# Optimization experiments

Measured on AMD Instinct MI355X. Metric: run time of the kernel, lower is better.

The kernel has to match this reference:

```python
import jax, jax.numpy as jnp
import numpy as np

N_NODES = 75000
N_EDGES = 1200000
IN_FEATS = 64
OUT_FEATS = 64


def setup_inputs() -> dict:
    key = jax.random.key(0)
    k1, k2, k3, k4, k5 = jax.random.split(key, 5)
    feature = jax.random.normal(k1, (N_NODES, IN_FEATS), dtype=jnp.float32)
    src = jax.random.randint(k2, (N_EDGES,), 0, N_NODES, dtype=jnp.int32)
    dst = jax.random.randint(k3, (N_EDGES,), 0, N_NODES, dtype=jnp.int32)
    # degree: in-degree + 1 (clamped >= 1 so sqrt/div are well-defined), float32 node data
    deg = np.bincount(np.asarray(dst), minlength=N_NODES).astype(np.float32) + 1.0
    degree = jnp.asarray(deg)
    W = jax.random.normal(k4, (IN_FEATS, OUT_FEATS), dtype=jnp.float32) * (1.0 / np.sqrt(IN_FEATS))
    b = jax.random.normal(k5, (OUT_FEATS,), dtype=jnp.float32) * 0.01
    return {"feature": feature, "degree": degree, "src": src, "dst": dst, "W": W, "b": b}


def reference(feature, degree, src, dst, W, b):
    # message: m_e = h[src_e] / sqrt(degree[src_e])   -> [E, F]
    inv_sqrt_deg = 1.0 / jnp.sqrt(degree)
    m = feature[src] * inv_sqrt_deg[src][:, None]
    # reduce: sum messages into destination nodes      -> [N, F]
    agg = jax.ops.segment_sum(m, dst, num_segments=feature.shape[0])
    # node apply: h = (agg / sqrt(degree)) @ W + b     -> [N, O]
    h = agg * inv_sqrt_deg[:, None]
    return h @ W + b
```

## Files before the change

### kernel.cpp

```cpp
#include <hip/hip_runtime.h>

#define FEATS 64
#define PSZ   64
#define MAXP  1280
#define PSCH  2344
#define SPT   512
#define PEPT  5
#define NBMAX 512
#define CAPP  2560

typedef __attribute__((ext_vector_type(8))) short short8;
typedef __attribute__((ext_vector_type(4))) float floatx4;

static __device__ __forceinline__ unsigned short f2bf(float f) {
    const unsigned int u = __float_as_uint(f);
    return (unsigned short)((u + 0x7FFFu + ((u >> 16) & 1u)) >> 16);
}
static __device__ __forceinline__ float bflo(unsigned int u) {
    return __uint_as_float(u << 16);
}
static __device__ __forceinline__ float bfhi(unsigned int u) {
    return __uint_as_float(u & 0xFFFF0000u);
}

__global__ __launch_bounds__(SPT) void prep_scatter(
        const float* __restrict__ degree,
        const float* __restrict__ feature,
        const float* __restrict__ Wm,
        const int* __restrict__ src,
        const int* __restrict__ dst,
        unsigned short* __restrict__ Fs16,
        unsigned short* __restrict__ WtB,
        int* __restrict__ slab,
        unsigned short* __restrict__ runoff,
        int n_nodes, int n_edges, int np, int rows_per) {
    __shared__ int cnt[MAXP];
    __shared__ int ssum[SPT];
    __shared__ int sval[PSCH];
    const int tid = threadIdx.x;
    const int b = blockIdx.x;

    for (int i = tid; i < np; i += SPT) cnt[i] = 0;

    {
        const int r0 = b * rows_per;
        const int r1 = min(r0 + rows_per, n_nodes);
        for (int idx = r0 * FEATS + tid; idx < r1 * FEATS; idx += SPT) {
            const float w = rsqrtf(degree[idx >> 6]);
            Fs16[idx] = f2bf(feature[idx] * w);
        }
        if (b == 0) {
            if (tid < FEATS) Fs16[(size_t)n_nodes * FEATS + tid] = 0;
            for (int idx = tid; idx < FEATS * FEATS; idx += SPT) {
                const int k = idx >> 6, n = idx & 63;
                WtB[n * FEATS + k] = f2bf(Wm[idx]);
            }
        }
    }
    __syncthreads();

    const int estart = b * PSCH;
    const int eend = min(estart + PSCH, n_edges);
    const int mb = eend - estart;

    int prk[PEPT];
#pragma unroll
    for (int k = 0; k < PEPT; ++k) {
        const int e = estart + tid + k * SPT;
        prk[k] = 0;
        if (e < eend) {
            const int d = dst[e];
            const int p = d >> 6;
            const int r = atomicAdd(&cnt[p], 1);
            prk[k] = p | (r << 11) | ((d & 63) << 23);
        }
    }
    __syncthreads();

    int my[3];
    int psum = 0;
    const int p0 = tid * 3;
#pragma unroll
    for (int j = 0; j < 3; ++j) {
        const int p = p0 + j;
        my[j] = psum;
        if (p < np) psum += cnt[p];
    }
    ssum[tid] = psum;
    __syncthreads();
#pragma unroll
    for (int o = 1; o < SPT; o <<= 1) {
        const int v = (tid >= o) ? ssum[tid - o] : 0;
        __syncthreads();
        ssum[tid] += v;
        __syncthreads();
    }
    const int tbase = ssum[tid] - psum;
#pragma unroll
    for (int j = 0; j < 3; ++j) {
        const int p = p0 + j;
        if (p < np) cnt[p] = tbase + my[j];
    }
    __syncthreads();

#pragma unroll
    for (int k = 0; k < PEPT; ++k) {
        const int e = estart + tid + k * SPT;
        if (e < eend) {
            const int pr = prk[k];
            const int p = pr & 2047;
            const int r = (pr >> 11) & 4095;
            const int dl = (pr >> 23) & 63;
            sval[cnt[p] + r] = (src[e] & 0x1FFFF) | (dl << 17);
        }
    }
    __syncthreads();

    int* so = slab + estart;
    for (int i = tid; i < mb; i += SPT) so[i] = sval[i];
    unsigned short* ro = runoff + (size_t)b * (np + 1);
    for (int i = tid; i <= np; i += SPT)
        ro[i] = (unsigned short)((i < np) ? cnt[i] : mb);
}

__global__ __launch_bounds__(256) void gather_apply5(
        const int* __restrict__ slab,
        const unsigned short* __restrict__ runoff,
        const float* __restrict__ degree,
        const unsigned short* __restrict__ Fs16,
        const unsigned short* __restrict__ WtB,
        const float* __restrict__ bias,
        float* __restrict__ out,
        int n_nodes, int np, int nbs) {
    __shared__ __align__(16) int ledges[CAPP];
    __shared__ __align__(16) unsigned short saggb[PSZ * 72];
    __shared__ int boffA[PSZ + 1];
    __shared__ int bcnt[PSZ];
    __shared__ int bcur[PSZ];
    __shared__ float swinv[PSZ];

    const int tid = threadIdx.x;
    const int lane = tid & 63;
    const int wv = tid >> 6;
    const int p = blockIdx.x;
    const int n0 = p * PSZ;
    const int nn = min(PSZ, n_nodes - n0);

    if (tid < PSZ) bcur[tid] = 0;
    if (wv == 0) {
        const float dg = (lane < nn) ? degree[n0 + lane] : 1.0f;
        swinv[lane] = rsqrtf(dg);
        const int c = (lane < nn) ? ((int)(dg + 0.5f) - 1) : 0;
        const int cp = (c + 7) & ~7;
        int x = cp;
#pragma unroll
        for (int off = 1; off < 64; off <<= 1) {
            const int v = __shfl_up(x, off);
            if (lane >= off) x += v;
        }
        if (lane == 0) boffA[0] = 0;
        boffA[lane + 1] = x;
        bcnt[lane] = c;
    }
    __syncthreads();
    const int mpad = boffA[PSZ];
    const uint2* FsU2 = (const uint2*)Fs16;

    if (mpad <= CAPP) {
        for (int i = tid; i < mpad; i += 256) ledges[i] = n_nodes;
        __syncthreads();
        for (int rr = tid; rr < nbs; rr += 256) {
            const unsigned short* ro = runoff + (size_t)rr * (np + 1);
            const int st = ro[p];
            const int en = ro[p + 1];
            const int* g = slab + (size_t)rr * PSCH;
            for (int q = st; q < en; ++q) {
                const int rec = g[q];
                const int dl = (rec >> 17) & 63;
                const int pos = boffA[dl] + atomicAdd(&bcur[dl], 1);
                ledges[pos] = rec & 0x1FFFF;
            }
        }
        __syncthreads();

        const int q4 = lane >> 4;
        const int c16 = lane & 15;
        for (int n = wv; n < PSZ; n += 4) {
            const int st = boffA[n];
            const int en8 = boffA[n + 1];
            float a0 = 0.f, a1 = 0.f, a2 = 0.f, a3 = 0.f;
            float c0 = 0.f, c1 = 0.f, c2 = 0.f, c3 = 0.f;
#pragma unroll 2
            for (int j = st; j < en8; j += 8) {
                const int r0 = ledges[j + q4];
                const int r1 = ledges[j + 4 + q4];
                const uint2 u0 = FsU2[((size_t)r0 << 4) + c16];
                const uint2 u1 = FsU2[((size_t)r1 << 4) + c16];
                a0 += bflo(u0.x); a1 += bfhi(u0.x);
                a2 += bflo(u0.y); a3 += bfhi(u0.y);
                c0 += bflo(u1.x); c1 += bfhi(u1.x);
                c2 += bflo(u1.y); c3 += bfhi(u1.y);
            }
            float v0 = a0 + c0, v1 = a1 + c1, v2 = a2 + c2, v3 = a3 + c3;
            v0 += __shfl(v0, lane ^ 16); v0 += __shfl(v0, lane ^ 32);
            v1 += __shfl(v1, lane ^ 16); v1 += __shfl(v1, lane ^ 32);
            v2 += __shfl(v2, lane ^ 16); v2 += __shfl(v2, lane ^ 32);
            v3 += __shfl(v3, lane ^ 16); v3 += __shfl(v3, lane ^ 32);
            if (q4 == 0) {
                const unsigned int pk0 =
                    (unsigned int)f2bf(v0) | ((unsigned int)f2bf(v1) << 16);
                const unsigned int pk1 =
                    (unsigned int)f2bf(v2) | ((unsigned int)f2bf(v3) << 16);
                uint2* dp = (uint2*)(saggb + n * 72 + c16 * 4);
                *dp = make_uint2(pk0, pk1);
            }
        }
    } else {
        __syncthreads();
        __syncthreads();
        for (int n = wv; n < PSZ; n += 4) {
            float acc = 0.f;
            for (int t = 0; t < nbs; ++t) {
                const unsigned short* ro = runoff + (size_t)t * (np + 1);
                const int gb = t * PSCH;
                const int e0 = ro[p + 1];
                for (int i = ro[p]; i < e0; ++i) {
                    const int rec = slab[gb + i];
                    if (((rec >> 17) & 63) == n) {
                        const unsigned int us =
                            Fs16[((size_t)(rec & 0x1FFFF) << 6) + lane];
                        acc += __uint_as_float(us << 16);
                    }
                }
            }
            saggb[n * 72 + lane] = f2bf(acc);
        }
    }
    __syncthreads();

    const int col = lane & 15;
    const int quad = lane >> 4;
    floatx4 acc[4] = {};
#pragma unroll
    for (int kt = 0; kt < 2; ++kt) {
        const short8 af = *(const short8*)(saggb + (wv * 16 + col) * 72 + kt * 32 + quad * 8);
#pragma unroll
        for (int nt = 0; nt < 4; ++nt) {
            const short8 bf = *(const short8*)((const short*)WtB + (nt * 16 + col) * FEATS + kt * 32 + quad * 8);
            acc[nt] = __builtin_amdgcn_mfma_f32_16x16x32_bf16(af, bf, acc[nt], 0, 0, 0);
        }
    }
#pragma unroll
    for (int nt = 0; nt < 4; ++nt) {
        const float bv = bias[nt * 16 + col];
#pragma unroll
        for (int r = 0; r < 4; ++r) {
            const int row = wv * 16 + quad * 4 + r;
            if (row < nn)
                out[(size_t)(n0 + row) * FEATS + nt * 16 + col] = swinv[row] * acc[nt][r] + bv;
        }
    }
}

static inline size_t align256(size_t x) { return (x + 255) & ~(size_t)255; }

extern "C" void kernel_launch(void* const* d_in, const int* in_sizes, int n_in,
                              void* d_out, int out_size, void* d_ws, size_t ws_size,
                              hipStream_t stream) {
    const float* feature = (const float*)d_in[0];
    const float* degree  = (const float*)d_in[1];
    const int*   src     = (const int*)d_in[2];
    const int*   dst     = (const int*)d_in[3];
    const float* Wm      = (const float*)d_in[4];
    const float* bias    = (const float*)d_in[5];
    float* out = (float*)d_out;

    const int n_nodes = in_sizes[1];
    const int n_edges = in_sizes[2];
    const int np = (n_nodes + PSZ - 1) / PSZ;
    const int nbs = (n_edges + PSCH - 1) / PSCH;
    const int rows_per = (n_nodes + nbs - 1) / nbs;

    char* ws = (char*)d_ws;
    unsigned short* Fs16 = (unsigned short*)ws; ws += align256(((size_t)n_nodes + 1) * FEATS * 2);
    unsigned short* WtB  = (unsigned short*)ws; ws += align256((size_t)FEATS * FEATS * 2);
    int* slab = (int*)ws;                       ws += align256((size_t)nbs * PSCH * 4);
    unsigned short* runoff = (unsigned short*)ws; ws += align256((size_t)nbs * (np + 1) * 2);

    prep_scatter<<<nbs, SPT, 0, stream>>>(degree, feature, Wm, src, dst,
                                          Fs16, WtB, slab, runoff,
                                          n_nodes, n_edges, np, rows_per);
    gather_apply5<<<np, 256, 0, stream>>>(slab, runoff, degree, Fs16, WtB, bias, out,
                                          n_nodes, np, nbs);
}
```

Measured before the change: 133.9 us.

## Use wave-shuffle scan in scatter and 16-byte row loads in gather

The prep kernel now computes its block-wide prefix sum with a wavefront shuffle scan plus per-wave totals. This replaces a shared-memory Hillis-Steele scan that needed many barriers. It also packs src into the per-edge register record so src is not read a second time. The gather kernel loads each neighbour row with 8 lanes of uint4 (16 bytes) instead of 16 lanes of uint2, so 8 edges are covered per wave iteration. That needs a longer shuffle reduction and uses a single accumulator set instead of two interleaved ones.

New measurement: 143.2 us. 7.0% more time.

```diff
diff --git a/kernel.cpp b/kernel.cpp
--- a/kernel.cpp
+++ b/kernel.cpp
@@ -2,7 +2,7 @@
 
 #define FEATS 64
 #define PSZ   64
-#define MAXP  1280
+#define MAXP  1536
 #define PSCH  2344
 #define SPT   512
 #define PEPT  5
@@ -35,9 +35,11 @@
         unsigned short* __restrict__ runoff,
         int n_nodes, int n_edges, int np, int rows_per) {
     __shared__ int cnt[MAXP];
-    __shared__ int ssum[SPT];
+    __shared__ int wtot[SPT / 64];
     __shared__ int sval[PSCH];
     const int tid = threadIdx.x;
+    const int lane = tid & 63;
+    const int wv = tid >> 6;
     const int b = blockIdx.x;
 
     for (int i = tid; i < np; i += SPT) cnt[i] = 0;
@@ -63,7 +65,7 @@
     const int eend = min(estart + PSCH, n_edges);
     const int mb = eend - estart;
 
-    int prk[PEPT];
+    unsigned long long prk[PEPT];
 #pragma unroll
     for (int k = 0; k < PEPT; ++k) {
         const int e = estart + tid + k * SPT;
@@ -72,46 +74,45 @@
             const int d = dst[e];
             const int p = d >> 6;
             const int r = atomicAdd(&cnt[p], 1);
-            prk[k] = p | (r << 11) | ((d & 63) << 23);
-        }
-    }
-    __syncthreads();
-
-    int my[3];
-    int psum = 0;
+            prk[k] = (unsigned long long)(src[e] & 0x1FFFF)
+                   | ((unsigned long long)(d & 63) << 17)
+                   | ((unsigned long long)p << 23)
+                   | ((unsigned long long)r << 34);
+        }
+    }
+    __syncthreads();
+
     const int p0 = tid * 3;
-#pragma unroll
-    for (int j = 0; j < 3; ++j) {
-        const int p = p0 + j;
-        my[j] = psum;
-        if (p < np) psum += cnt[p];
-    }
-    ssum[tid] = psum;
-    __syncthreads();
-#pragma unroll
-    for (int o = 1; o < SPT; o <<= 1) {
-        const int v = (tid >= o) ? ssum[tid - o] : 0;
-        __syncthreads();
-        ssum[tid] += v;
-        __syncthreads();
-    }
-    const int tbase = ssum[tid] - psum;
-#pragma unroll
-    for (int j = 0; j < 3; ++j) {
-        const int p = p0 + j;
-        if (p < np) cnt[p] = tbase + my[j];
-    }
+    int c0 = 0, c1 = 0, c2 = 0;
+    if (p0 + 0 < np) c0 = cnt[p0 + 0];
+    if (p0 + 1 < np) c1 = cnt[p0 + 1];
+    if (p0 + 2 < np) c2 = cnt[p0 + 2];
+    const int s = c0 + c1 + c2;
+    int incl = s;
+#pragma unroll
+    for (int o = 1; o < 64; o <<= 1) {
+        const int v = __shfl_up(incl, o);
+        if (lane >= o) incl += v;
+    }
+    if (lane == 63) wtot[wv] = incl;
+    __syncthreads();
+    int woff = 0;
+#pragma unroll
+    for (int j = 0; j < SPT / 64; ++j) woff += (j < wv) ? wtot[j] : 0;
+    const int tbase = woff + incl - s;
+    if (p0 + 0 < np) cnt[p0 + 0] = tbase;
+    if (p0 + 1 < np) cnt[p0 + 1] = tbase + c0;
+    if (p0 + 2 < np) cnt[p0 + 2] = tbase + c0 + c1;
     __syncthreads();
 
 #pragma unroll
     for (int k = 0; k < PEPT; ++k) {
         const int e = estart + tid + k * SPT;
         if (e < eend) {
-            const int pr = prk[k];
-            const int p = pr & 2047;
-            const int r = (pr >> 11) & 4095;
-            const int dl = (pr >> 23) & 63;
-            sval[cnt[p] + r] = (src[e] & 0x1FFFF) | (dl << 17);
+            const unsigned long long pr = prk[k];
+            const int p = (int)(pr >> 23) & 2047;
+            const int r = (int)(pr >> 34);
+            sval[cnt[p] + r] = (int)(pr & 0x7FFFFF);
         }
     }
     __syncthreads();
@@ -123,7 +124,7 @@
         ro[i] = (unsigned short)((i < np) ? cnt[i] : mb);
 }
 
-__global__ __launch_bounds__(256) void gather_apply5(
+__global__ __launch_bounds__(256) void gather_apply6(
         const int* __restrict__ slab,
         const unsigned short* __restrict__ runoff,
         const float* __restrict__ degree,
@@ -135,7 +136,6 @@
     __shared__ __align__(16) int ledges[CAPP];
     __shared__ __align__(16) unsigned short saggb[PSZ * 72];
     __shared__ int boffA[PSZ + 1];
-    __shared__ int bcnt[PSZ];
     __shared__ int bcur[PSZ];
     __shared__ float swinv[PSZ];
 
@@ -160,11 +160,10 @@
         }
         if (lane == 0) boffA[0] = 0;
         boffA[lane + 1] = x;
-        bcnt[lane] = c;
     }
     __syncthreads();
     const int mpad = boffA[PSZ];
-    const uint2* FsU2 = (const uint2*)Fs16;
+    const uint4* FsU4 = (const uint4*)Fs16;
 
     if (mpad <= CAPP) {
         for (int i = tid; i < mpad; i += 256) ledges[i] = n_nodes;
@@ -183,36 +182,40 @@
         }
         __syncthreads();
 
-        const int q4 = lane >> 4;
-        const int c16 = lane & 15;
+        const int q8 = lane >> 3;
+        const int c8 = lane & 7;
         for (int n = wv; n < PSZ; n += 4) {
             const int st = boffA[n];
             const int en8 = boffA[n + 1];
             float a0 = 0.f, a1 = 0.f, a2 = 0.f, a3 = 0.f;
-            float c0 = 0.f, c1 = 0.f, c2 = 0.f, c3 = 0.f;
+            float a4 = 0.f, a5 = 0.f, a6 = 0.f, a7 = 0.f;
 #pragma unroll 2
             for (int j = st; j < en8; j += 8) {
-                const int r0 = ledges[j + q4];
-                const int r1 = ledges[j + 4 + q4];
-                const uint2 u0 = FsU2[((size_t)r0 << 4) + c16];
-                const uint2 u1 = FsU2[((size_t)r1 << 4) + c16];
-                a0 += bflo(u0.x); a1 += bfhi(u0.x);
-                a2 += bflo(u0.y); a3 += bfhi(u0.y);
-                c0 += bflo(u1.x); c1 += bfhi(u1.x);
-                c2 += bflo(u1.y); c3 += bfhi(u1.y);
-            }
-            float v0 = a0 + c0, v1 = a1 + c1, v2 = a2 + c2, v3 = a3 + c3;
-            v0 += __shfl(v0, lane ^ 16); v0 += __shfl(v0, lane ^ 32);
-            v1 += __shfl(v1, lane ^ 16); v1 += __shfl(v1, lane ^ 32);
-            v2 += __shfl(v2, lane ^ 16); v2 += __shfl(v2, lane ^ 32);
-            v3 += __shfl(v3, lane ^ 16); v3 += __shfl(v3, lane ^ 32);
-            if (q4 == 0) {
-                const unsigned int pk0 =
-                    (unsigned int)f2bf(v0) | ((unsigned int)f2bf(v1) << 16);
-                const unsigned int pk1 =
-                    (unsigned int)f2bf(v2) | ((unsigned int)f2bf(v3) << 16);
-                uint2* dp = (uint2*)(saggb + n * 72 + c16 * 4);
-                *dp = make_uint2(pk0, pk1);
+                const int r0 = ledges[j + q8];
+                const uint4 u = FsU4[((size_t)r0 << 3) + c8];
+                a0 += bflo(u.x); a1 += bfhi(u.x);
+                a2 += bflo(u.y); a3 += bfhi(u.y);
+                a4 += bflo(u.z); a5 += bfhi(u.z);
+                a6 += bflo(u.w); a7 += bfhi(u.w);
+            }
+#pragma unroll
+            for (int o = 8; o < 64; o <<= 1) {
+                a0 += __shfl(a0, lane ^ o);
+                a1 += __shfl(a1, lane ^ o);
+                a2 += __shfl(a2, lane ^ o);
+                a3 += __shfl(a3, lane ^ o);
+                a4 += __shfl(a4, lane ^ o);
+                a5 += __shfl(a5, lane ^ o);
+                a6 += __shfl(a6, lane ^ o);
+                a7 += __shfl(a7, lane ^ o);
+            }
+            if (q8 == 0) {
+                uint4 pk;
+                pk.x = (unsigned int)f2bf(a0) | ((unsigned int)f2bf(a1) << 16);
+                pk.y = (unsigned int)f2bf(a2) | ((unsigned int)f2bf(a3) << 16);
+                pk.z = (unsigned int)f2bf(a4) | ((unsigned int)f2bf(a5) << 16);
+                pk.w = (unsigned int)f2bf(a6) | ((unsigned int)f2bf(a7) << 16);
+                *(uint4*)(saggb + n * 72 + c8 * 8) = pk;
             }
         }
     } else {
@@ -290,6 +293,6 @@
     prep_scatter<<<nbs, SPT, 0, stream>>>(degree, feature, Wm, src, dst,
                                           Fs16, WtB, slab, runoff,
                                           n_nodes, n_edges, np, rows_per);
-    gather_apply5<<<np, 256, 0, stream>>>(slab, runoff, degree, Fs16, WtB, bias, out,
+    gather_apply6<<<np, 256, 0, stream>>>(slab, runoff, degree, Fs16, WtB, bias, out,
                                           n_nodes, np, nbs);
 }
```

## Halve scatter block size and chunk, use wave-shuffle scan, pack src early

Applied to the files above, without the earlier changes.

The prep_scatter kernel now runs 256-thread blocks over 1172-edge chunks, which doubles the number of blocks and the number of runoff rows the gather kernel must walk. The 512-wide shared-memory prefix scan, with two barriers per step, is replaced by a per-thread 5-partition serial sum, a wave-level __shfl_up scan and a small per-wave totals array. The src load moves into the first pass and is packed into a 64-bit record, so the second pass no longer re-reads src. This trades more, smaller blocks and more segments per partition in gather_apply5 for fewer barriers and better occupancy in the scatter phase. An unused bcnt array is also removed.

Result: slower. 137.5 us (+2.7%).

```diff
diff --git a/kernel.cpp b/kernel.cpp
--- a/kernel.cpp
+++ b/kernel.cpp
@@ -3,10 +3,10 @@
 #define FEATS 64
 #define PSZ   64
 #define MAXP  1280
-#define PSCH  2344
-#define SPT   512
+#define PSCH  1172
+#define SPT   256
 #define PEPT  5
-#define NBMAX 512
+#define NBMAX 1024
 #define CAPP  2560
 
 typedef __attribute__((ext_vector_type(8))) short short8;
@@ -35,9 +35,11 @@
         unsigned short* __restrict__ runoff,
         int n_nodes, int n_edges, int np, int rows_per) {
     __shared__ int cnt[MAXP];
-    __shared__ int ssum[SPT];
+    __shared__ int wtot[SPT / 64];
     __shared__ int sval[PSCH];
     const int tid = threadIdx.x;
+    const int lane = tid & 63;
+    const int wv = tid >> 6;
     const int b = blockIdx.x;
 
     for (int i = tid; i < np; i += SPT) cnt[i] = 0;
@@ -63,7 +65,7 @@
     const int eend = min(estart + PSCH, n_edges);
     const int mb = eend - estart;
 
-    int prk[PEPT];
+    unsigned long long prk[PEPT];
 #pragma unroll
     for (int k = 0; k < PEPT; ++k) {
         const int e = estart + tid + k * SPT;
@@ -72,32 +74,39 @@
             const int d = dst[e];
             const int p = d >> 6;
             const int r = atomicAdd(&cnt[p], 1);
-            prk[k] = p | (r << 11) | ((d & 63) << 23);
-        }
-    }
-    __syncthreads();
-
-    int my[3];
-    int psum = 0;
-    const int p0 = tid * 3;
-#pragma unroll
-    for (int j = 0; j < 3; ++j) {
+            prk[k] = (unsigned long long)(src[e] & 0x1FFFF)
+                   | ((unsigned long long)(d & 63) << 17)
+                   | ((unsigned long long)p << 23)
+                   | ((unsigned long long)r << 34);
+        }
+    }
+    __syncthreads();
+
+    const int p0 = tid * 5;
+    int c[5];
+    int my[5];
+    int s = 0;
+#pragma unroll
+    for (int j = 0; j < 5; ++j) {
         const int p = p0 + j;
-        my[j] = psum;
-        if (p < np) psum += cnt[p];
-    }
-    ssum[tid] = psum;
-    __syncthreads();
-#pragma unroll
-    for (int o = 1; o < SPT; o <<= 1) {
-        const int v = (tid >= o) ? ssum[tid - o] : 0;
-        __syncthreads();
-        ssum[tid] += v;
-        __syncthreads();
-    }
-    const int tbase = ssum[tid] - psum;
-#pragma unroll
-    for (int j = 0; j < 3; ++j) {
+        c[j] = (p < np) ? cnt[p] : 0;
+        my[j] = s;
+        s += c[j];
+    }
+    int incl = s;
+#pragma unroll
+    for (int o = 1; o < 64; o <<= 1) {
+        const int v = __shfl_up(incl, o);
+        if (lane >= o) incl += v;
+    }
+    if (lane == 63) wtot[wv] = incl;
+    __syncthreads();
+    int woff = 0;
+#pragma unroll
+    for (int j = 0; j < SPT / 64; ++j) woff += (j < wv) ? wtot[j] : 0;
+    const int tbase = woff + incl - s;
+#pragma unroll
+    for (int j = 0; j < 5; ++j) {
         const int p = p0 + j;
         if (p < np) cnt[p] = tbase + my[j];
     }
@@ -107,11 +116,10 @@
     for (int k = 0; k < PEPT; ++k) {
         const int e = estart + tid + k * SPT;
         if (e < eend) {
-            const int pr = prk[k];
-            const int p = pr & 2047;
-            const int r = (pr >> 11) & 4095;
-            const int dl = (pr >> 23) & 63;
-            sval[cnt[p] + r] = (src[e] & 0x1FFFF) | (dl << 17);
+            const unsigned long long pr = prk[k];
+            const int p = (int)(pr >> 23) & 2047;
+            const int r = (int)(pr >> 34);
+            sval[cnt[p] + r] = (int)(pr & 0x7FFFFF);
         }
     }
     __syncthreads();
@@ -135,7 +143,6 @@
     __shared__ __align__(16) int ledges[CAPP];
     __shared__ __align__(16) unsigned short saggb[PSZ * 72];
     __shared__ int boffA[PSZ + 1];
-    __shared__ int bcnt[PSZ];
     __shared__ int bcur[PSZ];
     __shared__ float swinv[PSZ];
 
@@ -160,7 +167,6 @@
         }
         if (lane == 0) boffA[0] = 0;
         boffA[lane + 1] = x;
-        bcnt[lane] = c;
     }
     __syncthreads();
     const int mpad = boffA[PSZ];
```
